# Kernel tuning notes

Hardware: AMD Instinct MI355X
Metric: run time of the kernel (lower is better)

## Reference

```python
import jax, jax.numpy as jnp
import numpy as np

N = 2_000_000   # points
B = 4           # batch
C = 32          # feature channels
H = 512         # image height (== round(K[0,0]))
W = 512         # image width
GRID = 64       # grid_resolution


def setup_inputs() -> dict:
    key = jax.random.key(0)
    k1, k2, k3 = jax.random.split(key, 3)
    bids = jax.random.randint(k1, (N, 1), 0, B)
    coords = jax.random.randint(k2, (N, 3), 0, GRID)
    dense_coords = jnp.concatenate([bids, coords], axis=1).astype(jnp.int32)  # [N,4]
    pixel_features = jax.random.normal(k3, (B, C, H, W), dtype=jnp.float32)
    K = jnp.array([[512.0, 0.0, 256.0],
                   [0.0, 512.0, 256.0],
                   [0.0, 0.0, 1.0]], dtype=jnp.float32)
    P = jnp.array([[1.0, 0.0, 0.0, 0.0],
                   [0.0, 1.0, 0.0, 0.0],
                   [0.0, 0.0, 1.0, 3.0],
                   [0.0, 0.0, 0.0, 1.0]], dtype=jnp.float32)
    return {"dense_coords": dense_coords, "pixel_features": pixel_features, "K": K, "P": P}


def reference(dense_coords, pixel_features, K, P):
    grid_res = GRID
    batch_ids = dense_coords[:, 0]
    grid_pos = dense_coords[:, 1:].astype(pixel_features.dtype)
    # grid coords -> world positions in [-1, 1]
    world = grid_pos * (2.0 / (grid_res - 1)) - 1.0  # [N,3]
    ones = jnp.ones((world.shape[0], 1), world.dtype)
    pts_h = jnp.concatenate([world, ones], axis=1)   # [N,4]
    # project: camera = P @ pts^T, normalize by homogeneous coord
    cam = pts_h @ P.T                                # [N,4]
    cam = cam / cam[:, 3:4]
    img_h = cam[:, :3] @ K.T                         # [N,3]
    img_h = img_h / img_h[:, 2:3]
    image_x = img_h[:, 0]   # js (columns)
    image_y = img_h[:, 1]   # is (rows)
    points_depth = cam[:, 2:3]                       # [N,1]

    i0f = jnp.floor(image_y)
    j0f = jnp.floor(image_x)
    di = (image_y - i0f)[:, None]                    # [N,1]
    dj = (image_x - j0f)[:, None]                    # [N,1]

    Hh = pixel_features.shape[2]
    Ww = pixel_features.shape[3]
    i0 = jnp.clip(i0f.astype(jnp.int32), 0, Hh - 1)
    i1 = jnp.clip(i0f.astype(jnp.int32) + 1, 0, Hh - 1)
    j0 = jnp.clip(j0f.astype(jnp.int32), 0, Ww - 1)
    j1 = jnp.clip(j0f.astype(jnp.int32) + 1, 0, Ww - 1)

    b = batch_ids
    # four gathers, each [N, C] (advanced indices split by ':' -> result dims first)
    f00 = pixel_features[b, :, i0, j0]
    f10 = pixel_features[b, :, i1, j0]
    f01 = pixel_features[b, :, i0, j1]
    f11 = pixel_features[b, :, i1, j1]

    mean_j = (1.0 - di) * f00 + di * f10
    mean_jp = (1.0 - di) * f01 + di * f11
    feature_bilinear = (1.0 - dj) * mean_j + dj * mean_jp  # [N,C]
    return feature_bilinear, points_depth
```

## Files before the change

kernel.cpp:

```cpp
#include <hip/hip_runtime.h>

#define GRID_RES 64
#define C_CH     32
#define H_IMG    512
#define W_IMG    512
#define NBINS    512

typedef float    f32x4 __attribute__((ext_vector_type(4)));
typedef int      i32x4 __attribute__((ext_vector_type(4)));
typedef unsigned u32x4 __attribute__((ext_vector_type(4)));

__device__ __forceinline__ ushort f32_to_bf16(float f) {
    union { float f; unsigned u; } a; a.f = f;
    unsigned r = (a.u + 0x7FFFu + ((a.u >> 16) & 1u)) >> 16;
    return (ushort)r;
}
__device__ __forceinline__ float bf16lo_to_f32(unsigned u) {
    union { unsigned u; float f; } a; a.u = u << 16; return a.f;
}
__device__ __forceinline__ float bf16hi_to_f32(unsigned u) {
    union { unsigned u; float f; } a; a.u = u & 0xFFFF0000u; return a.f;
}

struct ProjOut {
    int   base;
    int   dji;
    int   dii;
    float di, dj, depth;
    int   bin;
};
__device__ __forceinline__ ProjOut project_pt(
    const i32x4 cc, const float* __restrict__ Km, const float* __restrict__ Pm)
{
    const float s = 2.0f / (float)(GRID_RES - 1);
    float wx = (float)cc.y * s - 1.0f;
    float wy = (float)cc.z * s - 1.0f;
    float wz = (float)cc.w * s - 1.0f;

    float cam0 = Pm[0]  * wx + Pm[1]  * wy + Pm[2]  * wz + Pm[3];
    float cam1 = Pm[4]  * wx + Pm[5]  * wy + Pm[6]  * wz + Pm[7];
    float cam2 = Pm[8]  * wx + Pm[9]  * wy + Pm[10] * wz + Pm[11];
    float cam3 = Pm[12] * wx + Pm[13] * wy + Pm[14] * wz + Pm[15];
    cam0 /= cam3; cam1 /= cam3; cam2 /= cam3;

    float g0 = Km[0] * cam0 + Km[1] * cam1 + Km[2] * cam2;
    float g1 = Km[3] * cam0 + Km[4] * cam1 + Km[5] * cam2;
    float g2 = Km[6] * cam0 + Km[7] * cam1 + Km[8] * cam2;
    float image_x = g0 / g2;
    float image_y = g1 / g2;

    float i0f = floorf(image_y);
    float j0f = floorf(image_x);
    float di = image_y - i0f;
    float dj = image_x - j0f;
    i0f = fminf(fmaxf(i0f, -1.0e9f), 1.0e9f);
    j0f = fminf(fmaxf(j0f, -1.0e9f), 1.0e9f);
    int i0r = (int)i0f;
    int j0r = (int)j0f;
    int i0 = min(max(i0r,     0), H_IMG - 1);
    int i1 = min(max(i0r + 1, 0), H_IMG - 1);
    int j0 = min(max(j0r,     0), W_IMG - 1);
    int j1 = min(max(j0r + 1, 0), W_IMG - 1);
    int b  = cc.x;

    ProjOut o;
    o.base  = ((b * H_IMG + i0) * W_IMG + j0) * C_CH;
    o.dji   = (j1 - j0) * C_CH;
    o.dii   = (i1 - i0) * W_IMG * C_CH;
    o.di    = di;
    o.dj    = dj;
    o.depth = cam2;
    o.bin   = b * 128 + (i0 >> 5) * 8 + (j0 >> 6);
    return o;
}

__global__ __launch_bounds__(256) void transpose_bf16_kernel(
    const float* __restrict__ in, ushort* __restrict__ out)
{
    const int HW = H_IMG * W_IMG;
    __shared__ float tile[C_CH * 65];

    const int tilesPerBatch = HW / 64;
    const int b   = blockIdx.x / tilesPerBatch;
    const int t   = blockIdx.x % tilesPerBatch;
    const int hw0 = t * 64;
    const int tid = threadIdx.x;

    const int c_r = tid >> 3;
    const int u_r = (tid & 7) * 8;
    const f32x4* src = (const f32x4*)(in + ((size_t)(b * C_CH + c_r) * HW + hw0 + u_r));
    f32x4 v0 = __builtin_nontemporal_load(src);
    f32x4 v1 = __builtin_nontemporal_load(src + 1);
    float* d = &tile[c_r * 65 + u_r];
    d[0] = v0.x; d[1] = v0.y; d[2] = v0.z; d[3] = v0.w;
    d[4] = v1.x; d[5] = v1.y; d[6] = v1.z; d[7] = v1.w;

    __syncthreads();

    const int u_w = tid >> 2;
    const int c0  = (tid & 3) * 8;
    union { ushort us[8]; uint4 v; } pk;
#pragma unroll
    for (int k = 0; k < 8; ++k)
        pk.us[k] = f32_to_bf16(tile[(c0 + k) * 65 + u_w]);
    *(uint4*)(out + ((size_t)(b * HW + hw0 + u_w) * C_CH + c0)) = pk.v;
}

__global__ __launch_bounds__(512) void init_hist_kernel(int* __restrict__ hist)
{
    hist[threadIdx.x] = 0;
}

__global__ __launch_bounds__(256) void hist_kernel(
    const int* __restrict__ coords,
    const float* __restrict__ Km, const float* __restrict__ Pm,
    int* __restrict__ hist, int N)
{
    __shared__ int lh[NBINS];
    const int tid = threadIdx.x;
    for (int i = tid; i < NBINS; i += 256) lh[i] = 0;
    __syncthreads();

    for (int p = blockIdx.x * 256 + tid; p < N; p += gridDim.x * 256) {
        i32x4 cc = __builtin_nontemporal_load((const i32x4*)coords + p);
        ProjOut o = project_pt(cc, Km, Pm);
        atomicAdd(&lh[o.bin], 1);
    }
    __syncthreads();
    for (int i = tid; i < NBINS; i += 256)
        if (lh[i]) atomicAdd(&hist[i], lh[i]);
}

__global__ __launch_bounds__(512) void scan_kernel(
    const int* __restrict__ hist, int* __restrict__ cursor)
{
    __shared__ int tmp[NBINS];
    const int t = threadIdx.x;
    const int v = hist[t];
    tmp[t] = v;
    __syncthreads();
    for (int off = 1; off < NBINS; off <<= 1) {
        int a = (t >= off) ? tmp[t - off] : 0;
        __syncthreads();
        tmp[t] += a;
        __syncthreads();
    }
    cursor[t] = tmp[t] - v;
}

__global__ __launch_bounds__(1024) void scatter_kernel(
    const int* __restrict__ coords,
    const float* __restrict__ Km, const float* __restrict__ Pm,
    int* __restrict__ cursor,
    i32x4* __restrict__ records,
    float* __restrict__ out_depth, int N)
{
    __shared__ int lh[NBINS];
    __shared__ int lbase[NBINS];
    const int tid = threadIdx.x;
    const int p0  = blockIdx.x * 4096;

    for (int i = tid; i < NBINS; i += 1024) lh[i] = 0;
    __syncthreads();

    int      binA[4], rankA[4], baseA[4];
    unsigned pfA[4];
    float    diA[4], djA[4];
#pragma unroll
    for (int k = 0; k < 4; ++k) {
        const int pp = p0 + k * 1024 + tid;
        binA[k] = -1;
        if (pp < N) {
            i32x4 cc = __builtin_nontemporal_load((const i32x4*)coords + pp);
            ProjOut o = project_pt(cc, Km, Pm);
            binA[k]  = o.bin;
            baseA[k] = o.base;
            diA[k]   = o.di;
            djA[k]   = o.dj;
            pfA[k]   = (unsigned)pp
                     | ((unsigned)(o.dji != 0) << 30)
                     | ((unsigned)(o.dii != 0) << 31);
            rankA[k] = atomicAdd(&lh[o.bin], 1);
            __builtin_nontemporal_store(o.depth, out_depth + pp);
        }
    }
    __syncthreads();

    for (int i = tid; i < NBINS; i += 1024) {
        int c = lh[i];
        if (c) lbase[i] = atomicAdd(&cursor[i], c);
    }
    __syncthreads();

#pragma unroll
    for (int k = 0; k < 4; ++k) {
        if (binA[k] >= 0) {
            const int slot = lbase[binA[k]] + rankA[k];
            i32x4 rec;
            rec.x = baseA[k];
            rec.y = (int)pfA[k];
            rec.z = __float_as_int(diA[k]);
            rec.w = __float_as_int(djA[k]);
            records[slot] = rec;
        }
    }
}

__global__ __launch_bounds__(256) void gather_sorted_kernel(
    const i32x4*  __restrict__ records,
    const ushort* __restrict__ feat,
    float* __restrict__ out_feat,
    int N, int swz_q, int swz_r)
{
    const int orig = blockIdx.x;
    const int xcd  = orig & 7;
    const int idx  = orig >> 3;
    const int wg   = (xcd < swz_r ? xcd * (swz_q + 1)
                                  : swz_r * (swz_q + 1) + (xcd - swz_r) * swz_q) + idx;
    const int s0   = wg * 256;

    __shared__ int   s_base[256];
    __shared__ unsigned s_pf[256];
    __shared__ float s_di[256];
    __shared__ float s_dj[256];

    const int tid = threadIdx.x;
    if (s0 + tid < N) {
        i32x4 rec = __builtin_nontemporal_load(records + s0 + tid);
        s_base[tid] = rec.x;
        s_pf[tid]   = (unsigned)rec.y;
        s_di[tid]   = __int_as_float(rec.z);
        s_dj[tid]   = __int_as_float(rec.w);
    }
    __syncthreads();

    const int cq   = tid & 3;
    const int slot = tid >> 2;
#pragma unroll
    for (int it = 0; it < 4; ++it) {
        const int lp = it * 64 + slot;
        if (s0 + lp < N) {
            const unsigned pf  = s_pf[lp];
            const int   base = s_base[lp] + cq * 8;
            const int   dji  = (int)((pf >> 30) & 1u) << 5;
            const int   dii  = (int)((pf >> 31) & 1u) << 14;
            const int   pidx = (int)(pf & 0x3FFFFFFFu);
            const float fdi  = s_di[lp];
            const float fdj  = s_dj[lp];

            const u32x4 u00 = *(const u32x4*)(feat + base);
            const u32x4 u01 = *(const u32x4*)(feat + base + dji);
            const u32x4 u10 = *(const u32x4*)(feat + base + dii);
            const u32x4 u11 = *(const u32x4*)(feat + base + dii + dji);

            float o[8];
            const unsigned* a00 = (const unsigned*)&u00;
            const unsigned* a01 = (const unsigned*)&u01;
            const unsigned* a10 = (const unsigned*)&u10;
            const unsigned* a11 = (const unsigned*)&u11;
#pragma unroll
            for (int k = 0; k < 4; ++k) {
                float f00 = bf16lo_to_f32(a00[k]), f01 = bf16lo_to_f32(a01[k]);
                float f10 = bf16lo_to_f32(a10[k]), f11 = bf16lo_to_f32(a11[k]);
                float r0 = f00 + fdi * (f10 - f00);
                float r1 = f01 + fdi * (f11 - f01);
                o[2 * k] = r0 + fdj * (r1 - r0);
                f00 = bf16hi_to_f32(a00[k]); f01 = bf16hi_to_f32(a01[k]);
                f10 = bf16hi_to_f32(a10[k]); f11 = bf16hi_to_f32(a11[k]);
                r0 = f00 + fdi * (f10 - f00);
                r1 = f01 + fdi * (f11 - f01);
                o[2 * k + 1] = r0 + fdj * (r1 - r0);
            }
            float* op = out_feat + (size_t)pidx * C_CH + cq * 8;
            f32x4 lo4 = { o[0], o[1], o[2], o[3] };
            f32x4 hi4 = { o[4], o[5], o[6], o[7] };
            __builtin_nontemporal_store(lo4, (f32x4*)op);
            __builtin_nontemporal_store(hi4, (f32x4*)(op + 4));
        }
    }
}

__global__ __launch_bounds__(256) void gather_bf16_kernel(
    const int*    __restrict__ coords,
    const ushort* __restrict__ feat,
    const float*  __restrict__ Km,
    const float*  __restrict__ Pm,
    float* __restrict__ out_feat,
    float* __restrict__ out_depth,
    int N)
{
    __shared__ int   s_base[256];
    __shared__ int   s_dji[256];
    __shared__ int   s_dii[256];
    __shared__ float s_fdi[256];
    __shared__ float s_fdj[256];

    const int tid = threadIdx.x;
    const int p0  = blockIdx.x * 256;

    {
        const int p = p0 + tid;
        if (p < N) {
            i32x4 cc = __builtin_nontemporal_load((const i32x4*)coords + p);
            ProjOut o = project_pt(cc, Km, Pm);
            s_base[tid] = o.base;
            s_dji[tid]  = o.dji;
            s_dii[tid]  = o.dii;
            s_fdi[tid]  = o.di;
            s_fdj[tid]  = o.dj;
            __builtin_nontemporal_store(o.depth, out_depth + p);
        }
    }
    __syncthreads();

    const int cq   = tid & 3;
    const int slot = tid >> 2;
#pragma unroll
    for (int it = 0; it < 4; ++it) {
        const int lp = it * 64 + slot;
        const int p  = p0 + lp;
        if (p < N) {
            const int   base = s_base[lp] + cq * 8;
            const int   dji  = s_dji[lp];
            const int   dii  = s_dii[lp];
            const float fdi  = s_fdi[lp];
            const float fdj  = s_fdj[lp];

            const u32x4 u00 = *(const u32x4*)(feat + base);
            const u32x4 u01 = *(const u32x4*)(feat + base + dji);
            const u32x4 u10 = *(const u32x4*)(feat + base + dii);
            const u32x4 u11 = *(const u32x4*)(feat + base + dii + dji);

            float o[8];
            const unsigned* a00 = (const unsigned*)&u00;
            const unsigned* a01 = (const unsigned*)&u01;
            const unsigned* a10 = (const unsigned*)&u10;
            const unsigned* a11 = (const unsigned*)&u11;
#pragma unroll
            for (int k = 0; k < 4; ++k) {
                float f00 = bf16lo_to_f32(a00[k]), f01 = bf16lo_to_f32(a01[k]);
                float f10 = bf16lo_to_f32(a10[k]), f11 = bf16lo_to_f32(a11[k]);
                float r0 = f00 + fdi * (f10 - f00);
                float r1 = f01 + fdi * (f11 - f01);
                o[2 * k] = r0 + fdj * (r1 - r0);
                f00 = bf16hi_to_f32(a00[k]); f01 = bf16hi_to_f32(a01[k]);
                f10 = bf16hi_to_f32(a10[k]); f11 = bf16hi_to_f32(a11[k]);
                r0 = f00 + fdi * (f10 - f00);
                r1 = f01 + fdi * (f11 - f01);
                o[2 * k + 1] = r0 + fdj * (r1 - r0);
            }
            float* op = out_feat + (size_t)p * C_CH + cq * 8;
            f32x4 lo4 = { o[0], o[1], o[2], o[3] };
            f32x4 hi4 = { o[4], o[5], o[6], o[7] };
            __builtin_nontemporal_store(lo4, (f32x4*)op);
            __builtin_nontemporal_store(hi4, (f32x4*)(op + 4));
        }
    }
}

__global__ __launch_bounds__(64) void gather_fp32_direct_kernel(
    const int*   __restrict__ coords,
    const float* __restrict__ feat,
    const float* __restrict__ Km,
    const float* __restrict__ Pm,
    float* __restrict__ out_feat,
    float* __restrict__ out_depth,
    int N)
{
    const int tid = threadIdx.x;
    const int p0  = blockIdx.x * 2;
    const int HW  = H_IMG * W_IMG;

    __shared__ int   s_base[2];
    __shared__ int   s_dji[2];
    __shared__ int   s_dii[2];
    __shared__ float s_fdi[2];
    __shared__ float s_fdj[2];

    if (tid < 2) {
        const int p = p0 + tid;
        if (p < N) {
            i32x4 cc = ((const i32x4*)coords)[p];
            const float s = 2.0f / (float)(GRID_RES - 1);
            float wx = (float)cc.y * s - 1.0f;
            float wy = (float)cc.z * s - 1.0f;
            float wz = (float)cc.w * s - 1.0f;
            float cam0 = Pm[0]  * wx + Pm[1]  * wy + Pm[2]  * wz + Pm[3];
            float cam1 = Pm[4]  * wx + Pm[5]  * wy + Pm[6]  * wz + Pm[7];
            float cam2 = Pm[8]  * wx + Pm[9]  * wy + Pm[10] * wz + Pm[11];
            float cam3 = Pm[12] * wx + Pm[13] * wy + Pm[14] * wz + Pm[15];
            cam0 /= cam3; cam1 /= cam3; cam2 /= cam3;
            float g0 = Km[0] * cam0 + Km[1] * cam1 + Km[2] * cam2;
            float g1 = Km[3] * cam0 + Km[4] * cam1 + Km[5] * cam2;
            float g2 = Km[6] * cam0 + Km[7] * cam1 + Km[8] * cam2;
            float image_x = g0 / g2;
            float image_y = g1 / g2;
            float i0f = floorf(image_y);
            float j0f = floorf(image_x);
            float di = image_y - i0f;
            float dj = image_x - j0f;
            i0f = fminf(fmaxf(i0f, -1.0e9f), 1.0e9f);
            j0f = fminf(fmaxf(j0f, -1.0e9f), 1.0e9f);
            int i0r = (int)i0f;
            int j0r = (int)j0f;
            int i0 = min(max(i0r,     0), H_IMG - 1);
            int i1 = min(max(i0r + 1, 0), H_IMG - 1);
            int j0 = min(max(j0r,     0), W_IMG - 1);
            int j1 = min(max(j0r + 1, 0), W_IMG - 1);
            int b  = cc.x;
            s_base[tid] = (b * C_CH * H_IMG + i0) * W_IMG + j0;
            s_dji[tid]  = (j1 - j0);
            s_dii[tid]  = (i1 - i0) * W_IMG;
            s_fdi[tid]  = di;
            s_fdj[tid]  = dj;
            out_depth[p] = cam2;
        }
    }
    __syncthreads();

    const int c  = tid & 31;
    const int lp = tid >> 5;
    const int p  = p0 + lp;
    if (p < N) {
        const int   base = s_base[lp];
        const int   dji  = s_dji[lp];
        const int   dii  = s_dii[lp];
        const float fdi  = s_fdi[lp];
        const float fdj  = s_fdj[lp];
        const float* fp = feat + base + (size_t)c * HW;
        float f00 = fp[0];
        float f01 = fp[dji];
        float f10 = fp[dii];
        float f11 = fp[dii + dji];
        float r0 = f00 + fdi * (f10 - f00);
        float r1 = f01 + fdi * (f11 - f01);
        out_feat[(size_t)p * C_CH + c] = r0 + fdj * (r1 - r0);
    }
}

extern "C" void kernel_launch(void* const* d_in, const int* in_sizes, int n_in,
                              void* d_out, int out_size, void* d_ws, size_t ws_size,
                              hipStream_t stream)
{
    const int*   coords = (const int*)  d_in[0];
    const float* feat   = (const float*)d_in[1];
    const float* Km     = (const float*)d_in[2];
    const float* Pm     = (const float*)d_in[3];

    const int N  = in_sizes[0] / 4;
    const int HW = H_IMG * W_IMG;
    const int Bb = in_sizes[1] / (C_CH * HW);

    float* out_feat  = (float*)d_out;
    float* out_depth = out_feat + (size_t)N * C_CH;

    const size_t map_bytes  = (size_t)in_sizes[1] * sizeof(ushort);
    const size_t rec_bytes  = (size_t)N * 16;
    const size_t hist_bytes = NBINS * sizeof(int);
    const size_t need_full  = map_bytes + rec_bytes + 2 * hist_bytes + 256;

    if (ws_size >= need_full) {
        char* ws = (char*)d_ws;
        ushort* tfeat   = (ushort*)ws;                      ws += map_bytes;
        i32x4*  records = (i32x4*)ws;                       ws += rec_bytes;
        int*    hist    = (int*)ws;                         ws += hist_bytes;
        int*    cursor  = (int*)ws;

        const int nwg = (N + 255) / 256;
        const int swz_q = nwg / 8;
        const int swz_r = nwg % 8;

        transpose_bf16_kernel<<<Bb * (HW / 64), 256, 0, stream>>>(feat, tfeat);
        init_hist_kernel<<<1, NBINS, 0, stream>>>(hist);
        hist_kernel<<<2048, 256, 0, stream>>>(coords, Km, Pm, hist, N);
        scan_kernel<<<1, NBINS, 0, stream>>>(hist, cursor);
        scatter_kernel<<<(N + 4095) / 4096, 1024, 0, stream>>>(
            coords, Km, Pm, cursor, records, out_depth, N);
        gather_sorted_kernel<<<nwg, 256, 0, stream>>>(
            records, tfeat, out_feat, N, swz_q, swz_r);
    } else if (ws_size >= map_bytes) {
        ushort* tfeat = (ushort*)d_ws;
        transpose_bf16_kernel<<<Bb * (HW / 64), 256, 0, stream>>>(feat, tfeat);
        gather_bf16_kernel<<<(N + 255) / 256, 256, 0, stream>>>(
            coords, tfeat, Km, Pm, out_feat, out_depth, N);
    } else {
        gather_fp32_direct_kernel<<<(N + 1) / 2, 64, 0, stream>>>(
            coords, feat, Km, Pm, out_feat, out_depth, N);
    }
}
```

Baseline: 475.2 us.

## Fuse histogram and scan via last-block pattern, enlarge gather tiles

Merges the histogram and prefix-scan kernels into one launch, where the last block to finish (found through an atomic done-counter) performs the scan. The depth output moves from scatter into the histogram pass, the histogram grid drops to 1024 blocks, and record writes become nontemporal. The sorted gather now processes 1024 points per workgroup instead of 256. The aim is fewer launches and less per-workgroup overhead, at the cost of a serial tail scan inside one block and fewer, larger gather workgroups.

```diff
diff --git a/kernel.cpp b/kernel.cpp
--- a/kernel.cpp
+++ b/kernel.cpp
@@ -5,6 +5,7 @@
 #define H_IMG    512
 #define W_IMG    512
 #define NBINS    512
+#define GPTS     1024
 
 typedef float    f32x4 __attribute__((ext_vector_type(4)));
 typedef int      i32x4 __attribute__((ext_vector_type(4)));
@@ -106,46 +107,59 @@
     *(uint4*)(out + ((size_t)(b * HW + hw0 + u_w) * C_CH + c0)) = pk.v;
 }
 
-__global__ __launch_bounds__(512) void init_hist_kernel(int* __restrict__ hist)
-{
-    hist[threadIdx.x] = 0;
-}
-
-__global__ __launch_bounds__(256) void hist_kernel(
+__global__ __launch_bounds__(1024) void init_kernel(int* __restrict__ hist_done)
+{
+    if (threadIdx.x < NBINS + 1) hist_done[threadIdx.x] = 0;
+}
+
+__global__ __launch_bounds__(256) void hist_scan_kernel(
     const int* __restrict__ coords,
     const float* __restrict__ Km, const float* __restrict__ Pm,
-    int* __restrict__ hist, int N)
+    int* __restrict__ hist,
+    int* __restrict__ done_ctr,
+    int* __restrict__ cursor,
+    float* __restrict__ out_depth,
+    int N, int nblocks)
 {
     __shared__ int lh[NBINS];
     const int tid = threadIdx.x;
     for (int i = tid; i < NBINS; i += 256) lh[i] = 0;
     __syncthreads();
 
-    for (int p = blockIdx.x * 256 + tid; p < N; p += gridDim.x * 256) {
+    for (int p = blockIdx.x * 256 + tid; p < N; p += nblocks * 256) {
         i32x4 cc = __builtin_nontemporal_load((const i32x4*)coords + p);
         ProjOut o = project_pt(cc, Km, Pm);
         atomicAdd(&lh[o.bin], 1);
+        __builtin_nontemporal_store(o.depth, out_depth + p);
     }
     __syncthreads();
     for (int i = tid; i < NBINS; i += 256)
         if (lh[i]) atomicAdd(&hist[i], lh[i]);
-}
-
-__global__ __launch_bounds__(512) void scan_kernel(
-    const int* __restrict__ hist, int* __restrict__ cursor)
-{
-    __shared__ int tmp[NBINS];
-    const int t = threadIdx.x;
-    const int v = hist[t];
-    tmp[t] = v;
-    __syncthreads();
+
+    __threadfence();
+    __syncthreads();
+    __shared__ int is_last;
+    if (tid == 0) is_last = (atomicAdd(done_ctr, 1) == nblocks - 1);
+    __syncthreads();
+    if (!is_last) return;
+
+    __threadfence();
+    __shared__ int sc[2][NBINS];
+    int x0 = atomicAdd(&hist[tid], 0);
+    int x1 = atomicAdd(&hist[tid + 256], 0);
+    sc[0][tid] = x0;
+    sc[0][tid + 256] = x1;
+    __syncthreads();
+    int s = 0;
     for (int off = 1; off < NBINS; off <<= 1) {
-        int a = (t >= off) ? tmp[t - off] : 0;
+        const int i0 = tid, i1 = tid + 256;
+        sc[s ^ 1][i0] = sc[s][i0] + (i0 >= off ? sc[s][i0 - off] : 0);
+        sc[s ^ 1][i1] = sc[s][i1] + (i1 >= off ? sc[s][i1 - off] : 0);
+        s ^= 1;
         __syncthreads();
-        tmp[t] += a;
-        __syncthreads();
-    }
-    cursor[t] = tmp[t] - v;
+    }
+    cursor[tid]       = sc[s][tid]       - x0;
+    cursor[tid + 256] = sc[s][tid + 256] - x1;
 }
 
 __global__ __launch_bounds__(1024) void scatter_kernel(
@@ -153,7 +167,7 @@
     const float* __restrict__ Km, const float* __restrict__ Pm,
     int* __restrict__ cursor,
     i32x4* __restrict__ records,
-    float* __restrict__ out_depth, int N)
+    int N)
 {
     __shared__ int lh[NBINS];
     __shared__ int lbase[NBINS];
@@ -181,7 +195,6 @@
                      | ((unsigned)(o.dji != 0) << 30)
                      | ((unsigned)(o.dii != 0) << 31);
             rankA[k] = atomicAdd(&lh[o.bin], 1);
-            __builtin_nontemporal_store(o.depth, out_depth + pp);
         }
     }
     __syncthreads();
@@ -201,7 +214,7 @@
             rec.y = (int)pfA[k];
             rec.z = __float_as_int(diA[k]);
             rec.w = __float_as_int(djA[k]);
-            records[slot] = rec;
+            __builtin_nontemporal_store(rec, records + slot);
         }
     }
 }
@@ -217,30 +230,32 @@
     const int idx  = orig >> 3;
     const int wg   = (xcd < swz_r ? xcd * (swz_q + 1)
                                   : swz_r * (swz_q + 1) + (xcd - swz_r) * swz_q) + idx;
-    const int s0   = wg * 256;
-
-    __shared__ int   s_base[256];
-    __shared__ unsigned s_pf[256];
-    __shared__ float s_di[256];
-    __shared__ float s_dj[256];
+    const int s0   = wg * GPTS;
+
+    __shared__ int      s_base[GPTS];
+    __shared__ unsigned s_pf[GPTS];
+    __shared__ float    s_di[GPTS];
+    __shared__ float    s_dj[GPTS];
 
     const int tid = threadIdx.x;
-    if (s0 + tid < N) {
-        i32x4 rec = __builtin_nontemporal_load(records + s0 + tid);
-        s_base[tid] = rec.x;
-        s_pf[tid]   = (unsigned)rec.y;
-        s_di[tid]   = __int_as_float(rec.z);
-        s_dj[tid]   = __int_as_float(rec.w);
+    for (int k = tid; k < GPTS; k += 256) {
+        if (s0 + k < N) {
+            i32x4 rec = __builtin_nontemporal_load(records + s0 + k);
+            s_base[k] = rec.x;
+            s_pf[k]   = (unsigned)rec.y;
+            s_di[k]   = __int_as_float(rec.z);
+            s_dj[k]   = __int_as_float(rec.w);
+        }
     }
     __syncthreads();
 
     const int cq   = tid & 3;
     const int slot = tid >> 2;
 #pragma unroll
-    for (int it = 0; it < 4; ++it) {
+    for (int it = 0; it < GPTS / 64; ++it) {
         const int lp = it * 64 + slot;
         if (s0 + lp < N) {
-            const unsigned pf  = s_pf[lp];
+            const unsigned pf = s_pf[lp];
             const int   base = s_base[lp] + cq * 8;
             const int   dji  = (int)((pf >> 30) & 1u) << 5;
             const int   dii  = (int)((pf >> 31) & 1u) << 14;
@@ -456,26 +471,28 @@
 
     const size_t map_bytes  = (size_t)in_sizes[1] * sizeof(ushort);
     const size_t rec_bytes  = (size_t)N * 16;
-    const size_t hist_bytes = NBINS * sizeof(int);
-    const size_t need_full  = map_bytes + rec_bytes + 2 * hist_bytes + 256;
+    const size_t meta_bytes = (NBINS + 1 + NBINS) * sizeof(int);
+    const size_t need_full  = map_bytes + rec_bytes + meta_bytes + 256;
 
     if (ws_size >= need_full) {
         char* ws = (char*)d_ws;
         ushort* tfeat   = (ushort*)ws;                      ws += map_bytes;
         i32x4*  records = (i32x4*)ws;                       ws += rec_bytes;
-        int*    hist    = (int*)ws;                         ws += hist_bytes;
-        int*    cursor  = (int*)ws;
-
-        const int nwg = (N + 255) / 256;
+        int*    hist    = (int*)ws;
+        int*    done    = hist + NBINS;
+        int*    cursor  = done + 1;
+
+        const int nwg   = (N + GPTS - 1) / GPTS;
         const int swz_q = nwg / 8;
         const int swz_r = nwg % 8;
+        const int hist_blocks = 1024;
 
         transpose_bf16_kernel<<<Bb * (HW / 64), 256, 0, stream>>>(feat, tfeat);
-        init_hist_kernel<<<1, NBINS, 0, stream>>>(hist);
-        hist_kernel<<<2048, 256, 0, stream>>>(coords, Km, Pm, hist, N);
-        scan_kernel<<<1, NBINS, 0, stream>>>(hist, cursor);
+        init_kernel<<<1, 1024, 0, stream>>>(hist);
+        hist_scan_kernel<<<hist_blocks, 256, 0, stream>>>(
+            coords, Km, Pm, hist, done, cursor, out_depth, N, hist_blocks);
         scatter_kernel<<<(N + 4095) / 4096, 1024, 0, stream>>>(
-            coords, Km, Pm, cursor, records, out_depth, N);
+            coords, Km, Pm, cursor, records, N);
         gather_sorted_kernel<<<nwg, 256, 0, stream>>>(
             records, tfeat, out_feat, N, swz_q, swz_r);
     } else if (ws_size >= map_bytes) {
```

Result: slower. 594.1 us (+25.0%).
